# Kernel optimization log

Hardware: AMD Instinct MI355X
Metric: run time of the kernel (lower is better)

## Reference

```python
import jax, jax.numpy as jnp
import numpy as np

IN_DIM = 256
HID = 256
A = 32          # n_agents
NH = 4          # attention heads
HD = 16         # head_dim = attention_dim / heads
CV = 16         # comm_value_dim
TOPK = 8
NACT = 20
BS = 2048
NEG = -1e10


def _lin(key, out_d, in_d):
    k1, k2 = jax.random.split(key)
    s = 1.0 / np.sqrt(in_d)
    w = jax.random.uniform(k1, (out_d, in_d), jnp.float32, -s, s)
    b = jax.random.uniform(k2, (out_d,), jnp.float32, -s, s)
    return w, b


def setup_inputs() -> dict:
    key = jax.random.key(0)
    ks = jax.random.split(key, 12)
    inputs = jax.random.normal(ks[0], (BS * A, IN_DIM), jnp.float32)
    hidden_state = jax.random.normal(ks[1], (BS * A, HID), jnp.float32)
    fc1_w, fc1_b = _lin(ks[2], HID, IN_DIM)
    gru_w_ih, gru_b_ih = _lin(ks[3], 3 * HID, HID)
    gru_w_hh, gru_b_hh = _lin(ks[4], 3 * HID, HID)
    q_w, q_b = _lin(ks[5], NH * HD, HID)
    k_w, k_b = _lin(ks[6], NH * HD, HID)
    v_w, v_b = _lin(ks[7], NH * CV, HID)
    g_w, g_b = _lin(ks[8], NH, HID)
    p1_w, p1_b = _lin(ks[9], HID, HID + NH * CV)
    p2_w, p2_b = _lin(ks[10], NACT, HID)
    return {
        'inputs': inputs, 'hidden_state': hidden_state,
        'fc1_w': fc1_w, 'fc1_b': fc1_b,
        'gru_w_ih': gru_w_ih, 'gru_w_hh': gru_w_hh,
        'gru_b_ih': gru_b_ih, 'gru_b_hh': gru_b_hh,
        'q_w': q_w, 'q_b': q_b, 'k_w': k_w, 'k_b': k_b,
        'v_w': v_w, 'v_b': v_b, 'g_w': g_w, 'g_b': g_b,
        'p1_w': p1_w, 'p1_b': p1_b, 'p2_w': p2_w, 'p2_b': p2_b,
        'bs': BS,
    }


def _forward(inputs, hidden_state, fc1_w, fc1_b, gru_w_ih, gru_w_hh,
             gru_b_ih, gru_b_hh, q_w, q_b, k_w, k_b, v_w, v_b,
             g_w, g_b, p1_w, p1_b, p2_w, p2_b, bs):
    x = jax.nn.relu(inputs @ fc1_w.T + fc1_b)
    h_in = hidden_state.reshape(-1, HID)
    # torch GRUCell: gates ordered r, z, n
    gi = x @ gru_w_ih.T + gru_b_ih
    gh = h_in @ gru_w_hh.T + gru_b_hh
    gi_r, gi_z, gi_n = jnp.split(gi, 3, axis=-1)
    gh_r, gh_z, gh_n = jnp.split(gh, 3, axis=-1)
    r = jax.nn.sigmoid(gi_r + gh_r)
    z = jax.nn.sigmoid(gi_z + gh_z)
    n = jnp.tanh(gi_n + r * gh_n)
    h = (1.0 - z) * n + z * h_in

    ah = h.reshape(bs, A, HID)                      # agent_hidden
    q = (ah @ q_w.T + q_b).reshape(bs, A, NH, HD)
    k = (ah @ k_w.T + k_b).reshape(bs, A, NH, HD)
    v = (ah @ v_w.T + v_b).reshape(bs, A, NH, CV)

    scores = jnp.einsum('bqhd,bkhd->bqkh', q, k) / np.sqrt(HD)  # [bs,A,A,NH]
    eye = jnp.eye(A, dtype=bool)[None, :, :, None]
    scores = jnp.where(eye, NEG, scores)

    # topk mask along neighbor dim (k < A-1 so mask is applied)
    sp = scores.transpose(0, 1, 3, 2)               # [bs,A,NH,A]
    _, idx = jax.lax.top_k(sp, TOPK)
    keep = jax.nn.one_hot(idx, A, dtype=jnp.float32).sum(axis=-2) > 0
    sp = jnp.where(keep, sp, NEG)
    sparse_scores = sp.transpose(0, 1, 3, 2)        # [bs,A,A,NH]

    alpha = jax.nn.softmax(sparse_scores, axis=2)
    head_messages = jnp.einsum('bqkh,bkhv->bqhv', alpha, v)  # [bs,A,NH,CV]
    gates = jax.nn.sigmoid(ah @ g_w.T + g_b)[..., None]      # [bs,A,NH,1]
    gated = head_messages * gates

    policy_in = jnp.concatenate([ah, gated.reshape(bs, A, NH * CV)], axis=-1)
    policy_in = policy_in.reshape(bs * A, HID + NH * CV)
    logits = jax.nn.relu(policy_in @ p1_w.T + p1_b) @ p2_w.T + p2_b
    return logits, h


def reference(inputs, hidden_state, fc1_w, fc1_b, gru_w_ih, gru_w_hh,
              gru_b_ih, gru_b_hh, q_w, q_b, k_w, k_b, v_w, v_b,
              g_w, g_b, p1_w, p1_b, p2_w, p2_b, bs):
    return _forward(inputs, hidden_state, fc1_w, fc1_b, gru_w_ih, gru_w_hh,
                    gru_b_ih, gru_b_hh, q_w, q_b, k_w, k_b, v_w, v_b,
                    g_w, g_b, p1_w, p1_b, p2_w, p2_b, bs)
```

## Files before the change

### kernel.cpp

```cpp
#include <hip/hip_runtime.h>
#include <hip/hip_bf16.h>
#include <math.h>

#define NBATCH 2048
#define NAG 32
#define HIDD 256
#define INDIM 256
#define PIN 320
#define NACTN 20
#define NEGV -1e10f
#define MT 64
#define NROWS (NBATCH*NAG)

typedef __attribute__((ext_vector_type(8))) __bf16 bf16x8;
typedef __attribute__((ext_vector_type(4))) float f32x4;

#define WO_W1   0
#define WO_WIH  65536
#define WO_WHH  262144
#define WO_WQ   458752
#define WO_WK   475136
#define WO_WV   491520
#define WO_WG   507904
#define WO_WP1  508928
#define WO_WP2  590848
#define WSO_Q   1048576
#define WSO_K   (WSO_Q + NROWS*64)
#define WSO_V   (WSO_K + NROWS*64)
#define WSO_G   (WSO_V + NROWS*64)

__device__ __forceinline__ unsigned short f2bf(float f) {
    union { float f; unsigned int i; } x; x.f = f;
    unsigned int r = x.i + 0x7fffu + ((x.i >> 16) & 1u);
    return (unsigned short)(r >> 16);
}
__device__ __forceinline__ float bf2f(unsigned short u) {
    union { unsigned int i; float f; } x; x.i = ((unsigned int)u) << 16; return x.f;
}
__device__ __forceinline__ float frcp(float x) { return __builtin_amdgcn_rcpf(x); }
__device__ __forceinline__ float sigm(float x) { return frcp(1.0f + __expf(-x)); }
__device__ __forceinline__ float tanh_fast(float x) {
    float e = __expf(2.0f * x);
    return 1.0f - 2.0f * frcp(e + 1.0f);
}

__device__ __forceinline__ int swz(int row, int col) {
    return row*256 + ((((col >> 3)) ^ (row & 7)) << 3) + (col & 7);
}
__device__ __forceinline__ int swzf(int row, int frag) {
    return row*256 + ((frag ^ (row & 7)) << 3);
}
__device__ __forceinline__ int swz64(int row, int col) {
    return row*64 + ((((col >> 3)) ^ (row & 7)) << 3) + (col & 7);
}
__device__ __forceinline__ int swzf64(int row, int frag) {
    return row*64 + ((frag ^ (row & 7)) << 3);
}

__device__ __forceinline__ bf16x8 ldfrag(const unsigned short* p) {
    return *(const bf16x8*)(const void*)p;
}
union ZU { uint4 u; bf16x8 v; };
__device__ __forceinline__ bf16x8 zfrag() {
    ZU x; x.u = make_uint4(0u, 0u, 0u, 0u); return x.v;
}
#define MFMA(a,b,c) __builtin_amdgcn_mfma_f32_16x16x32_bf16(a,b,c,0,0,0)

__global__ void __launch_bounds__(256)
convert_weights(const float* __restrict__ W1,  const float* __restrict__ Wih,
                const float* __restrict__ Whh, const float* __restrict__ Wq,
                const float* __restrict__ Wk,  const float* __restrict__ Wv,
                const float* __restrict__ Wg,  const float* __restrict__ Wp1,
                const float* __restrict__ Wp2, unsigned short* __restrict__ dst)
{
    int b = (int)blockIdx.x;
    const float* src; int base;
    if      (b <  64) { src = W1;  base = WO_W1;              }
    else if (b < 256) { src = Wih; base = WO_WIH; b -=  64;   }
    else if (b < 448) { src = Whh; base = WO_WHH; b -= 256;   }
    else if (b < 464) { src = Wq;  base = WO_WQ;  b -= 448;   }
    else if (b < 480) { src = Wk;  base = WO_WK;  b -= 464;   }
    else if (b < 496) { src = Wv;  base = WO_WV;  b -= 480;   }
    else if (b < 497) { src = Wg;  base = WO_WG;  b -= 496;   }
    else if (b < 577) { src = Wp1; base = WO_WP1; b -= 497;   }
    else              { src = Wp2; base = WO_WP2; b -= 577;   }
    const int idx = b * 1024 + (int)threadIdx.x * 4;
    float4 v = *(const float4*)(const void*)(src + idx);
    ushort4 u;
    u.x = f2bf(v.x); u.y = f2bf(v.y); u.z = f2bf(v.z); u.w = f2bf(v.w);
    *(ushort4*)(void*)(dst + base + idx) = u;
}

__global__ void __launch_bounds__(256, 2)
k1_gru_qkvg(const float* __restrict__ gIn, const float* __restrict__ gH,
            const unsigned short* __restrict__ wsW,
            const float* __restrict__ B1,
            const float* __restrict__ Bih, const float* __restrict__ Bhh,
            const float* __restrict__ Bq,  const float* __restrict__ Bk,
            const float* __restrict__ Bv,  const float* __restrict__ Bg,
            float* __restrict__ outH,
            unsigned short* __restrict__ wsQ, unsigned short* __restrict__ wsK,
            unsigned short* __restrict__ wsV, unsigned short* __restrict__ wsG)
{
    __shared__ __align__(16) unsigned short lA[MT*256];
    __shared__ __align__(16) unsigned short lB[MT*256];

    const unsigned short* W1  = wsW + WO_W1;
    const unsigned short* Wih = wsW + WO_WIH;
    const unsigned short* Whh = wsW + WO_WHH;
    const unsigned short* Wq  = wsW + WO_WQ;
    const unsigned short* Wk  = wsW + WO_WK;
    const unsigned short* Wv  = wsW + WO_WV;
    const unsigned short* Wg  = wsW + WO_WG;

    const int tid  = (int)threadIdx.x;
    const int lane = tid & 63;
    const int wv   = tid >> 6;
    const int l15  = lane & 15;
    const int quad = lane >> 4;
    const long rowBase = (long)blockIdx.x * MT;

    #pragma unroll
    for (int i = 0; i < 16; ++i) {
        const int job  = i*256 + tid;
        const int frag = job & 31;
        const int row  = (job >> 5) & 63;
        const int buf  = job >> 11;
        const float* src = (buf ? gH : gIn) + (rowBase + row)*256 + frag*8;
        float4 v0 = *(const float4*)(const void*)(src);
        float4 v1 = *(const float4*)(const void*)(src + 4);
        uint4 pk;
        pk.x = ((unsigned int)f2bf(v0.y) << 16) | f2bf(v0.x);
        pk.y = ((unsigned int)f2bf(v0.w) << 16) | f2bf(v0.z);
        pk.z = ((unsigned int)f2bf(v1.y) << 16) | f2bf(v1.x);
        pk.w = ((unsigned int)f2bf(v1.w) << 16) | f2bf(v1.z);
        unsigned short* dst = buf ? lB : lA;
        *(uint4*)(void*)(dst + swzf(row, frag)) = pk;
    }
    __syncthreads();

    f32x4 xa[4][4];
    #pragma unroll
    for (int i4 = 0; i4 < 4; ++i4) {
        const int nt = i4*4 + wv;
        const int n  = nt*16 + l15;
        f32x4 a0 = {0.f,0.f,0.f,0.f}, a1 = {0.f,0.f,0.f,0.f};
        f32x4 a2 = {0.f,0.f,0.f,0.f}, a3 = {0.f,0.f,0.f,0.f};
        #pragma unroll
        for (int kt = 0; kt < 8; ++kt) {
            const int frag = kt*4 + quad;
            bf16x8 bw = ldfrag(W1 + n*INDIM + frag*8);
            a0 = MFMA(ldfrag(lA + swzf(     l15, frag)), bw, a0);
            a1 = MFMA(ldfrag(lA + swzf(16 + l15, frag)), bw, a1);
            a2 = MFMA(ldfrag(lA + swzf(32 + l15, frag)), bw, a2);
            a3 = MFMA(ldfrag(lA + swzf(48 + l15, frag)), bw, a3);
        }
        const float b = B1[n];
        #pragma unroll
        for (int r = 0; r < 4; ++r) {
            a0[r] = fmaxf(a0[r] + b, 0.f); a1[r] = fmaxf(a1[r] + b, 0.f);
            a2[r] = fmaxf(a2[r] + b, 0.f); a3[r] = fmaxf(a3[r] + b, 0.f);
        }
        xa[i4][0] = a0; xa[i4][1] = a1; xa[i4][2] = a2; xa[i4][3] = a3;
    }
    __syncthreads();
    #pragma unroll
    for (int i4 = 0; i4 < 4; ++i4) {
        const int nt = i4*4 + wv;
        #pragma unroll
        for (int m = 0; m < 4; ++m) {
            #pragma unroll
            for (int r = 0; r < 4; ++r)
                lA[swz(m*16 + quad*4 + r, nt*16 + l15)] = f2bf(xa[i4][m][r]);
        }
    }
    __syncthreads();

    for (int jt = wv; jt < 16; jt += 4) {
        const int n = jt*16 + l15;
        f32x4 ir[4], iz[4], in_[4], hr[4], hz[4], hn[4];
        #pragma unroll
        for (int m = 0; m < 4; ++m) {
            ir[m] = (f32x4){0.f,0.f,0.f,0.f}; iz[m] = (f32x4){0.f,0.f,0.f,0.f};
            in_[m]= (f32x4){0.f,0.f,0.f,0.f}; hr[m] = (f32x4){0.f,0.f,0.f,0.f};
            hz[m] = (f32x4){0.f,0.f,0.f,0.f}; hn[m] = (f32x4){0.f,0.f,0.f,0.f};
        }
        #pragma unroll 2
        for (int kt = 0; kt < 8; ++kt) {
            const int frag = kt*4 + quad;
            const int k0 = frag*8;
            bf16x8 ax[4], ah[4];
            #pragma unroll
            for (int m = 0; m < 4; ++m) {
                ax[m] = ldfrag(lA + swzf(m*16 + l15, frag));
                ah[m] = ldfrag(lB + swzf(m*16 + l15, frag));
            }
            bf16x8 br = ldfrag(Wih + (n      )*HIDD + k0);
            bf16x8 bz = ldfrag(Wih + (n + 256)*HIDD + k0);
            bf16x8 bn = ldfrag(Wih + (n + 512)*HIDD + k0);
            bf16x8 cr = ldfrag(Whh + (n      )*HIDD + k0);
            bf16x8 cz = ldfrag(Whh + (n + 256)*HIDD + k0);
            bf16x8 cn = ldfrag(Whh + (n + 512)*HIDD + k0);
            #pragma unroll
            for (int m = 0; m < 4; ++m) {
                ir[m] = MFMA(ax[m], br, ir[m]);
                iz[m] = MFMA(ax[m], bz, iz[m]);
                in_[m]= MFMA(ax[m], bn, in_[m]);
                hr[m] = MFMA(ah[m], cr, hr[m]);
                hz[m] = MFMA(ah[m], cz, hz[m]);
                hn[m] = MFMA(ah[m], cn, hn[m]);
            }
        }
        const float bir_ = Bih[n], biz_ = Bih[n+256], bin_ = Bih[n+512];
        const float bhr_ = Bhh[n], bhz_ = Bhh[n+256], bhn_ = Bhh[n+512];
        #pragma unroll
        for (int m = 0; m < 4; ++m) {
            #pragma unroll
            for (int r = 0; r < 4; ++r) {
                const int row = m*16 + quad*4 + r;
                const float hprev = bf2f(lB[swz(row, n)]);
                const float rr = sigm(ir[m][r] + bir_ + hr[m][r] + bhr_);
                const float zz = sigm(iz[m][r] + biz_ + hz[m][r] + bhz_);
                const float nn = tanh_fast(in_[m][r] + bin_ + rr*(hn[m][r] + bhn_));
                outH[(rowBase + row)*HIDD + n] = (1.0f - zz)*nn + zz*hprev;
            }
        }
    }
    __syncthreads();

    #pragma unroll
    for (int i = 0; i < 8; ++i) {
        const int job  = i*256 + tid;
        const int frag = job & 31;
        const int row  = job >> 5;
        const float* src = outH + (rowBase + row)*256 + frag*8;
        float4 v0 = *(const float4*)(const void*)(src);
        float4 v1 = *(const float4*)(const void*)(src + 4);
        uint4 pk;
        pk.x = ((unsigned int)f2bf(v0.y) << 16) | f2bf(v0.x);
        pk.y = ((unsigned int)f2bf(v0.w) << 16) | f2bf(v0.z);
        pk.z = ((unsigned int)f2bf(v1.y) << 16) | f2bf(v1.x);
        pk.w = ((unsigned int)f2bf(v1.w) << 16) | f2bf(v1.z);
        *(uint4*)(void*)(lA + swzf(row, frag)) = pk;
    }
    __syncthreads();

    for (int job = wv; job < 13; job += 4) {
        const unsigned short* W; const float* Bi; unsigned short* dst; int nb;
        if      (job < 4)  { W = Wq; Bi = Bq; dst = wsQ; nb = job;     }
        else if (job < 8)  { W = Wk; Bi = Bk; dst = wsK; nb = job - 4; }
        else if (job < 12) { W = Wv; Bi = Bv; dst = wsV; nb = job - 8; }
        else               { W = Wg; Bi = Bg; dst = wsG; nb = 0;       }
        const bool isg   = (job == 12);
        const bool valid = !isg || (l15 < 4);
        const int n = nb*16 + l15;
        f32x4 ac[4];
        #pragma unroll
        for (int m = 0; m < 4; ++m) ac[m] = (f32x4){0.f,0.f,0.f,0.f};
        #pragma unroll
        for (int kt = 0; kt < 8; ++kt) {
            const int frag = kt*4 + quad;
            bf16x8 bw = valid ? ldfrag(W + n*HIDD + frag*8) : zfrag();
            #pragma unroll
            for (int m = 0; m < 4; ++m)
                ac[m] = MFMA(ldfrag(lA + swzf(m*16 + l15, frag)), bw, ac[m]);
        }
        if (valid) {
            const float b = Bi[n];
            #pragma unroll
            for (int m = 0; m < 4; ++m) {
                #pragma unroll
                for (int r = 0; r < 4; ++r) {
                    const int row = m*16 + quad*4 + r;
                    const float v = ac[m][r] + b;
                    if (isg) dst[(rowBase + row)*4  + l15]          = f2bf(v);
                    else     dst[(rowBase + row)*64 + nb*16 + l15]  = f2bf(v);
                }
            }
        }
    }
}

#define QS 68
__global__ void __launch_bounds__(256, 2)
k23_attn_policy(const float* __restrict__ gHnew,
                const unsigned short* __restrict__ wsW,
                const unsigned short* __restrict__ wsQ,
                const unsigned short* __restrict__ wsK,
                const unsigned short* __restrict__ wsV,
                const unsigned short* __restrict__ wsG,
                const float* __restrict__ Bp1, const float* __restrict__ Bp2,
                float* __restrict__ outL)
{
    __shared__ __align__(16) unsigned short lH[MT*256];
    __shared__ __align__(16) unsigned short lP[MT*256];
    __shared__ __align__(16) unsigned short lM[MT*64];
    __shared__ __align__(16) unsigned short sG[2*32*4];

    const unsigned short* Wp1 = wsW + WO_WP1;
    const unsigned short* Wp2 = wsW + WO_WP2;

    const int tid  = (int)threadIdx.x;
    const int lane = tid & 63;
    const int wv   = tid >> 6;
    const int l15  = lane & 15;
    const int quad = lane >> 4;
    const long rowBase = (long)blockIdx.x * MT;
    const long b0 = (long)blockIdx.x * 2;

    #pragma unroll
    for (int i = 0; i < 8; ++i) {
        const int job  = i*256 + tid;
        const int frag = job & 31;
        const int row  = job >> 5;
        const float* src = gHnew + (rowBase + row)*256 + frag*8;
        float4 v0 = *(const float4*)(const void*)(src);
        float4 v1 = *(const float4*)(const void*)(src + 4);
        uint4 pk;
        pk.x = ((unsigned int)f2bf(v0.y) << 16) | f2bf(v0.x);
        pk.y = ((unsigned int)f2bf(v0.w) << 16) | f2bf(v0.z);
        pk.z = ((unsigned int)f2bf(v1.y) << 16) | f2bf(v1.x);
        pk.w = ((unsigned int)f2bf(v1.w) << 16) | f2bf(v1.z);
        *(uint4*)(void*)(lH + swzf(row, frag)) = pk;
    }
    #pragma unroll
    for (int i = 0; i < 12; ++i) {
        const int j  = i*256 + tid;
        const int b  = (j >= 1536) ? 1 : 0;
        const int jj = b ? (j - 1536) : j;
        const int mat = jj >> 9;
        const int e   = jj & 511;
        const int row = e >> 4, c4 = e & 15;
        const unsigned short* srcm = (mat == 0) ? wsQ : (mat == 1) ? wsK : wsV;
        *(ushort4*)(void*)(lP + ((b*3 + mat)*32 + row)*QS + c4*4) =
            *(const ushort4*)(const void*)(srcm + ((b0 + b)*32 + row)*64 + c4*4);
    }
    if (tid < 64) {
        const int b = tid >> 5, row = tid & 31;
        *(ushort4*)(void*)(sG + (b*32 + row)*4) =
            *(const ushort4*)(const void*)(wsG + ((b0 + b)*32 + row)*4);
    }
    __syncthreads();

    {
        const int b  = tid >> 7;
        const int h  = (tid >> 5) & 3;
        const int qi = tid & 31;
        const unsigned short* q_ = lP + (b*3 + 0)*32*QS;
        const unsigned short* k_ = lP + (b*3 + 1)*32*QS;
        const unsigned short* v_ = lP + (b*3 + 2)*32*QS;

        float qv[16];
        #pragma unroll
        for (int c = 0; c < 16; ++c) qv[c] = bf2f(q_[qi*QS + h*16 + c]);
        float s0[32];
        #pragma unroll
        for (int ki = 0; ki < 32; ++ki) {
            float acc = 0.0f;
            #pragma unroll
            for (int c = 0; c < 16; ++c) acc += qv[c] * bf2f(k_[ki*QS + h*16 + c]);
            acc *= 0.25f;
            s0[ki] = (ki == qi) ? NEGV : acc;
        }
        unsigned int mask = 0u;
        float m1 = 0.0f;
        for (int t = 0; t < 8; ++t) {
            float best = -3.0e38f; int bidx = 0;
            #pragma unroll
            for (int i = 0; i < 32; ++i) {
                bool better = (((mask >> i) & 1u) == 0u) && (s0[i] > best);
                best = better ? s0[i] : best;
                bidx = better ? i : bidx;
            }
            mask |= (1u << bidx);
            if (t == 0) m1 = best;
        }
        float sum = 0.0f;
        #pragma unroll
        for (int i = 0; i < 32; ++i) {
            const float e = ((mask >> i) & 1u) ? __expf(s0[i] - m1) : 0.0f;
            s0[i] = e;
            sum += e;
        }
        const float inv = frcp(sum);
        const float gate = sigm(bf2f(sG[(b*32 + qi)*4 + h]));
        float msg[16];
        #pragma unroll
        for (int c = 0; c < 16; ++c) msg[c] = 0.0f;
        #pragma unroll
        for (int ki = 0; ki < 32; ++ki) {
            const float al = s0[ki] * inv;
            #pragma unroll
            for (int c = 0; c < 16; ++c) msg[c] += al * bf2f(v_[ki*QS + h*16 + c]);
        }
        const int mrow = b*32 + qi;
        #pragma unroll
        for (int c = 0; c < 16; ++c)
            lM[swz64(mrow, h*16 + c)] = f2bf(msg[c] * gate);
    }
    __syncthreads();

    #pragma unroll
    for (int i4 = 0; i4 < 4; ++i4) {
        const int nt = i4*4 + wv;
        const int n  = nt*16 + l15;
        f32x4 a0 = {0.f,0.f,0.f,0.f}, a1 = {0.f,0.f,0.f,0.f};
        f32x4 a2 = {0.f,0.f,0.f,0.f}, a3 = {0.f,0.f,0.f,0.f};
        #pragma unroll
        for (int kt = 0; kt < 10; ++kt) {
            bf16x8 bw = ldfrag(Wp1 + n*PIN + kt*32 + quad*8);
            bf16x8 f0, f1, f2, f3;
            if (kt < 8) {
                const int frag = kt*4 + quad;
                f0 = ldfrag(lH + swzf(     l15, frag));
                f1 = ldfrag(lH + swzf(16 + l15, frag));
                f2 = ldfrag(lH + swzf(32 + l15, frag));
                f3 = ldfrag(lH + swzf(48 + l15, frag));
            } else {
                const int frag = (kt - 8)*4 + quad;
                f0 = ldfrag(lM + swzf64(     l15, frag));
                f1 = ldfrag(lM + swzf64(16 + l15, frag));
                f2 = ldfrag(lM + swzf64(32 + l15, frag));
                f3 = ldfrag(lM + swzf64(48 + l15, frag));
            }
            a0 = MFMA(f0, bw, a0); a1 = MFMA(f1, bw, a1);
            a2 = MFMA(f2, bw, a2); a3 = MFMA(f3, bw, a3);
        }
        const float b = Bp1[n];
        #pragma unroll
        for (int r = 0; r < 4; ++r) {
            lP[swz(     quad*4 + r, n)] = f2bf(fmaxf(a0[r] + b, 0.f));
            lP[swz(16 + quad*4 + r, n)] = f2bf(fmaxf(a1[r] + b, 0.f));
            lP[swz(32 + quad*4 + r, n)] = f2bf(fmaxf(a2[r] + b, 0.f));
            lP[swz(48 + quad*4 + r, n)] = f2bf(fmaxf(a3[r] + b, 0.f));
        }
    }
    __syncthreads();

    for (int j = wv; j < 8; j += 4) {
        const int ntile = j >> 2, m = j & 3;
        const int n = ntile*16 + l15;
        const bool valid = (n < NACTN);
        f32x4 ac = {0.f,0.f,0.f,0.f};
        #pragma unroll
        for (int kt = 0; kt < 8; ++kt) {
            const int frag = kt*4 + quad;
            bf16x8 bw = valid ? ldfrag(Wp2 + n*HIDD + frag*8) : zfrag();
            ac = MFMA(ldfrag(lP + swzf(m*16 + l15, frag)), bw, ac);
        }
        if (valid) {
            const float b = Bp2[n];
            #pragma unroll
            for (int r = 0; r < 4; ++r)
                outL[(rowBase + m*16 + quad*4 + r)*NACTN + n] = ac[r] + b;
        }
    }
}

extern "C" void kernel_launch(void* const* d_in, const int* in_sizes, int n_in,
                              void* d_out, int out_size, void* d_ws, size_t ws_size,
                              hipStream_t stream) {
    (void)in_sizes; (void)n_in; (void)ws_size; (void)out_size;
    const float* gIn = (const float*)d_in[0];
    const float* gH  = (const float*)d_in[1];
    const float* W1  = (const float*)d_in[2];
    const float* B1  = (const float*)d_in[3];
    const float* Wih = (const float*)d_in[4];
    const float* Whh = (const float*)d_in[5];
    const float* Bih = (const float*)d_in[6];
    const float* Bhh = (const float*)d_in[7];
    const float* Wq  = (const float*)d_in[8];
    const float* Bq  = (const float*)d_in[9];
    const float* Wk  = (const float*)d_in[10];
    const float* Bk  = (const float*)d_in[11];
    const float* Wv  = (const float*)d_in[12];
    const float* Bv  = (const float*)d_in[13];
    const float* Wg  = (const float*)d_in[14];
    const float* Bg  = (const float*)d_in[15];
    const float* Wp1 = (const float*)d_in[16];
    const float* Bp1 = (const float*)d_in[17];
    const float* Wp2 = (const float*)d_in[18];
    const float* Bp2 = (const float*)d_in[19];
    float* outL = (float*)d_out;
    float* outH = outL + (size_t)NBATCH * NAG * NACTN;
    unsigned short* wsW = (unsigned short*)d_ws;

    hipLaunchKernelGGL(convert_weights, dim3(582), dim3(256), 0, stream,
        W1, Wih, Whh, Wq, Wk, Wv, Wg, Wp1, Wp2, wsW);
    hipLaunchKernelGGL(k1_gru_qkvg, dim3(NROWS/MT), dim3(256), 0, stream,
        gIn, gH, wsW, B1, Bih, Bhh, Bq, Bk, Bv, Bg,
        outH, wsW + WSO_Q, wsW + WSO_K, wsW + WSO_V, wsW + WSO_G);
    hipLaunchKernelGGL(k23_attn_policy, dim3(NROWS/MT), dim3(256), 0, stream,
        outH, wsW, wsW + WSO_Q, wsW + WSO_K, wsW + WSO_V, wsW + WSO_G,
        Bp1, Bp2, outL);
}
```

Measured before the change: 398.3 us.

## Fuse GRU/QKVG kernel with attention-policy kernel into one mega kernel

Merges the two main kernels so Q/K/V/G projections are written straight into shared memory instead of a global workspace. The attention and policy stages then run in the same block, reading h from the already-staged lA tile rather than reloading and reconverting outH. This removes the global round trip for QKVG and for h, plus one launch. In exchange it uses more shared memory per block (extra lM and sG buffers), which may lower occupancy, and it reuses lB across stages.

```diff
diff --git a/kernel.cpp b/kernel.cpp
--- a/kernel.cpp
+++ b/kernel.cpp
@@ -24,10 +24,6 @@
 #define WO_WG   507904
 #define WO_WP1  508928
 #define WO_WP2  590848
-#define WSO_Q   1048576
-#define WSO_K   (WSO_Q + NROWS*64)
-#define WSO_V   (WSO_K + NROWS*64)
-#define WSO_G   (WSO_V + NROWS*64)
 
 __device__ __forceinline__ unsigned short f2bf(float f) {
     union { float f; unsigned int i; } x; x.f = f;
@@ -91,19 +87,21 @@
     *(ushort4*)(void*)(dst + base + idx) = u;
 }
 
+#define QS 68
 __global__ void __launch_bounds__(256, 2)
-k1_gru_qkvg(const float* __restrict__ gIn, const float* __restrict__ gH,
-            const unsigned short* __restrict__ wsW,
-            const float* __restrict__ B1,
-            const float* __restrict__ Bih, const float* __restrict__ Bhh,
-            const float* __restrict__ Bq,  const float* __restrict__ Bk,
-            const float* __restrict__ Bv,  const float* __restrict__ Bg,
-            float* __restrict__ outH,
-            unsigned short* __restrict__ wsQ, unsigned short* __restrict__ wsK,
-            unsigned short* __restrict__ wsV, unsigned short* __restrict__ wsG)
+mega(const float* __restrict__ gIn, const float* __restrict__ gH,
+     const unsigned short* __restrict__ wsW,
+     const float* __restrict__ B1,
+     const float* __restrict__ Bih, const float* __restrict__ Bhh,
+     const float* __restrict__ Bq,  const float* __restrict__ Bk,
+     const float* __restrict__ Bv,  const float* __restrict__ Bg,
+     const float* __restrict__ Bp1, const float* __restrict__ Bp2,
+     float* __restrict__ outH, float* __restrict__ outL)
 {
     __shared__ __align__(16) unsigned short lA[MT*256];
     __shared__ __align__(16) unsigned short lB[MT*256];
+    __shared__ __align__(16) unsigned short lM[MT*64];
+    __shared__ __align__(16) unsigned short sG[2*32*4];
 
     const unsigned short* W1  = wsW + WO_W1;
     const unsigned short* Wih = wsW + WO_WIH;
@@ -112,6 +110,8 @@
     const unsigned short* Wk  = wsW + WO_WK;
     const unsigned short* Wv  = wsW + WO_WV;
     const unsigned short* Wg  = wsW + WO_WG;
+    const unsigned short* Wp1 = wsW + WO_WP1;
+    const unsigned short* Wp2 = wsW + WO_WP2;
 
     const int tid  = (int)threadIdx.x;
     const int lane = tid & 63;
@@ -246,11 +246,11 @@
     __syncthreads();
 
     for (int job = wv; job < 13; job += 4) {
-        const unsigned short* W; const float* Bi; unsigned short* dst; int nb;
-        if      (job < 4)  { W = Wq; Bi = Bq; dst = wsQ; nb = job;     }
-        else if (job < 8)  { W = Wk; Bi = Bk; dst = wsK; nb = job - 4; }
-        else if (job < 12) { W = Wv; Bi = Bv; dst = wsV; nb = job - 8; }
-        else               { W = Wg; Bi = Bg; dst = wsG; nb = 0;       }
+        const unsigned short* W; const float* Bi; int mat, nb;
+        if      (job < 4)  { W = Wq; Bi = Bq; mat = 0; nb = job;     }
+        else if (job < 8)  { W = Wk; Bi = Bk; mat = 1; nb = job - 4; }
+        else if (job < 12) { W = Wv; Bi = Bv; mat = 2; nb = job - 8; }
+        else               { W = Wg; Bi = Bg; mat = 3; nb = 0;       }
         const bool isg   = (job == 12);
         const bool valid = !isg || (l15 < 4);
         const int n = nb*16 + l15;
@@ -272,73 +272,13 @@
                 #pragma unroll
                 for (int r = 0; r < 4; ++r) {
                     const int row = m*16 + quad*4 + r;
+                    const int bb  = row >> 5, qi = row & 31;
                     const float v = ac[m][r] + b;
-                    if (isg) dst[(rowBase + row)*4  + l15]          = f2bf(v);
-                    else     dst[(rowBase + row)*64 + nb*16 + l15]  = f2bf(v);
+                    if (isg) sG[bb*128 + qi*4 + l15] = f2bf(v);
+                    else     lB[((bb*3 + mat)*32 + qi)*QS + nb*16 + l15] = f2bf(v);
                 }
             }
         }
-    }
-}
-
-#define QS 68
-__global__ void __launch_bounds__(256, 2)
-k23_attn_policy(const float* __restrict__ gHnew,
-                const unsigned short* __restrict__ wsW,
-                const unsigned short* __restrict__ wsQ,
-                const unsigned short* __restrict__ wsK,
-                const unsigned short* __restrict__ wsV,
-                const unsigned short* __restrict__ wsG,
-                const float* __restrict__ Bp1, const float* __restrict__ Bp2,
-                float* __restrict__ outL)
-{
-    __shared__ __align__(16) unsigned short lH[MT*256];
-    __shared__ __align__(16) unsigned short lP[MT*256];
-    __shared__ __align__(16) unsigned short lM[MT*64];
-    __shared__ __align__(16) unsigned short sG[2*32*4];
-
-    const unsigned short* Wp1 = wsW + WO_WP1;
-    const unsigned short* Wp2 = wsW + WO_WP2;
-
-    const int tid  = (int)threadIdx.x;
-    const int lane = tid & 63;
-    const int wv   = tid >> 6;
-    const int l15  = lane & 15;
-    const int quad = lane >> 4;
-    const long rowBase = (long)blockIdx.x * MT;
-    const long b0 = (long)blockIdx.x * 2;
-
-    #pragma unroll
-    for (int i = 0; i < 8; ++i) {
-        const int job  = i*256 + tid;
-        const int frag = job & 31;
-        const int row  = job >> 5;
-        const float* src = gHnew + (rowBase + row)*256 + frag*8;
-        float4 v0 = *(const float4*)(const void*)(src);
-        float4 v1 = *(const float4*)(const void*)(src + 4);
-        uint4 pk;
-        pk.x = ((unsigned int)f2bf(v0.y) << 16) | f2bf(v0.x);
-        pk.y = ((unsigned int)f2bf(v0.w) << 16) | f2bf(v0.z);
-        pk.z = ((unsigned int)f2bf(v1.y) << 16) | f2bf(v1.x);
-        pk.w = ((unsigned int)f2bf(v1.w) << 16) | f2bf(v1.z);
-        *(uint4*)(void*)(lH + swzf(row, frag)) = pk;
-    }
-    #pragma unroll
-    for (int i = 0; i < 12; ++i) {
-        const int j  = i*256 + tid;
-        const int b  = (j >= 1536) ? 1 : 0;
-        const int jj = b ? (j - 1536) : j;
-        const int mat = jj >> 9;
-        const int e   = jj & 511;
-        const int row = e >> 4, c4 = e & 15;
-        const unsigned short* srcm = (mat == 0) ? wsQ : (mat == 1) ? wsK : wsV;
-        *(ushort4*)(void*)(lP + ((b*3 + mat)*32 + row)*QS + c4*4) =
-            *(const ushort4*)(const void*)(srcm + ((b0 + b)*32 + row)*64 + c4*4);
-    }
-    if (tid < 64) {
-        const int b = tid >> 5, row = tid & 31;
-        *(ushort4*)(void*)(sG + (b*32 + row)*4) =
-            *(const ushort4*)(const void*)(wsG + ((b0 + b)*32 + row)*4);
     }
     __syncthreads();
 
@@ -346,9 +286,9 @@
         const int b  = tid >> 7;
         const int h  = (tid >> 5) & 3;
         const int qi = tid & 31;
-        const unsigned short* q_ = lP + (b*3 + 0)*32*QS;
-        const unsigned short* k_ = lP + (b*3 + 1)*32*QS;
-        const unsigned short* v_ = lP + (b*3 + 2)*32*QS;
+        const unsigned short* q_ = lB + (b*3 + 0)*32*QS;
+        const unsigned short* k_ = lB + (b*3 + 1)*32*QS;
+        const unsigned short* v_ = lB + (b*3 + 2)*32*QS;
 
         float qv[16];
         #pragma unroll
@@ -383,7 +323,7 @@
             sum += e;
         }
         const float inv = frcp(sum);
-        const float gate = sigm(bf2f(sG[(b*32 + qi)*4 + h]));
+        const float gate = sigm(bf2f(sG[b*128 + qi*4 + h]));
         float msg[16];
         #pragma unroll
         for (int c = 0; c < 16; ++c) msg[c] = 0.0f;
@@ -412,10 +352,10 @@
             bf16x8 f0, f1, f2, f3;
             if (kt < 8) {
                 const int frag = kt*4 + quad;
-                f0 = ldfrag(lH + swzf(     l15, frag));
-                f1 = ldfrag(lH + swzf(16 + l15, frag));
-                f2 = ldfrag(lH + swzf(32 + l15, frag));
-                f3 = ldfrag(lH + swzf(48 + l15, frag));
+                f0 = ldfrag(lA + swzf(     l15, frag));
+                f1 = ldfrag(lA + swzf(16 + l15, frag));
+                f2 = ldfrag(lA + swzf(32 + l15, frag));
+                f3 = ldfrag(lA + swzf(48 + l15, frag));
             } else {
                 const int frag = (kt - 8)*4 + quad;
                 f0 = ldfrag(lM + swzf64(     l15, frag));
@@ -429,10 +369,10 @@
         const float b = Bp1[n];
         #pragma unroll
         for (int r = 0; r < 4; ++r) {
-            lP[swz(     quad*4 + r, n)] = f2bf(fmaxf(a0[r] + b, 0.f));
-            lP[swz(16 + quad*4 + r, n)] = f2bf(fmaxf(a1[r] + b, 0.f));
-            lP[swz(32 + quad*4 + r, n)] = f2bf(fmaxf(a2[r] + b, 0.f));
-            lP[swz(48 + quad*4 + r, n)] = f2bf(fmaxf(a3[r] + b, 0.f));
+            lB[swz(     quad*4 + r, n)] = f2bf(fmaxf(a0[r] + b, 0.f));
+            lB[swz(16 + quad*4 + r, n)] = f2bf(fmaxf(a1[r] + b, 0.f));
+            lB[swz(32 + quad*4 + r, n)] = f2bf(fmaxf(a2[r] + b, 0.f));
+            lB[swz(48 + quad*4 + r, n)] = f2bf(fmaxf(a3[r] + b, 0.f));
         }
     }
     __syncthreads();
@@ -446,7 +386,7 @@
         for (int kt = 0; kt < 8; ++kt) {
             const int frag = kt*4 + quad;
             bf16x8 bw = valid ? ldfrag(Wp2 + n*HIDD + frag*8) : zfrag();
-            ac = MFMA(ldfrag(lP + swzf(m*16 + l15, frag)), bw, ac);
+            ac = MFMA(ldfrag(lB + swzf(m*16 + l15, frag)), bw, ac);
         }
         if (valid) {
             const float b = Bp2[n];
@@ -487,10 +427,6 @@
 
     hipLaunchKernelGGL(convert_weights, dim3(582), dim3(256), 0, stream,
         W1, Wih, Whh, Wq, Wk, Wv, Wg, Wp1, Wp2, wsW);
-    hipLaunchKernelGGL(k1_gru_qkvg, dim3(NROWS/MT), dim3(256), 0, stream,
-        gIn, gH, wsW, B1, Bih, Bhh, Bq, Bk, Bv, Bg,
-        outH, wsW + WSO_Q, wsW + WSO_K, wsW + WSO_V, wsW + WSO_G);
-    hipLaunchKernelGGL(k23_attn_policy, dim3(NROWS/MT), dim3(256), 0, stream,
-        outH, wsW, wsW + WSO_Q, wsW + WSO_K, wsW + WSO_V, wsW + WSO_G,
-        Bp1, Bp2, outL);
-}
+    hipLaunchKernelGGL(mega, dim3(NROWS/MT), dim3(256), 0, stream,
+        gIn, gH, wsW, B1, Bih, Bhh, Bq, Bk, Bv, Bg, Bp1, Bp2, outH, outL);
+}
```

Result: faster. 388.9 us (-2.4%).
